# Kernel tuning notes

Measured on AMD Instinct MI355X. Metric: run time of the kernel, lower is better.

## Reference

```python
import jax, jax.numpy as jnp
import numpy as np

B, N, K, C = 4, 8192, 16, 64
HID, OUT = 128, 128


def setup_inputs() -> dict:
    key = jax.random.key(0)
    ks = jax.random.split(key, 8)
    f = jax.random.normal(ks[0], (B, N, C), dtype=jnp.float32)
    knn_idx = jax.random.randint(ks[1], (B, N, K), 0, N, dtype=jnp.int32)
    W1 = jax.random.normal(ks[2], (3 * C, HID), dtype=jnp.float32) * (1.0 / np.sqrt(3 * C))
    b1 = jnp.zeros((HID,), dtype=jnp.float32)
    W2 = jax.random.normal(ks[3], (HID, HID), dtype=jnp.float32) * (1.0 / np.sqrt(HID))
    b2 = jnp.zeros((HID,), dtype=jnp.float32)
    W3 = jax.random.normal(ks[4], (HID, OUT), dtype=jnp.float32) * 0.05  # init.normal_(std=0.05)
    b3 = jnp.zeros((OUT,), dtype=jnp.float32)  # init.zeros_
    return {"f": f, "knn_idx": knn_idx, "W1": W1, "b1": b1, "W2": W2, "b2": b2, "W3": W3, "b3": b3}


def reference(f, knn_idx, W1, b1, W2, b2, W3, b3):
    # knn_group: gather neighbor features -> [B, N, k, C]
    knn_feat = jax.vmap(lambda fb, ib: fb[ib])(f, knn_idx)
    f_tiled = jnp.broadcast_to(f[:, :, None, :], knn_feat.shape)  # [B,N,k,C]
    x = jnp.concatenate([f_tiled, knn_feat, knn_feat - f_tiled], axis=-1)  # [B,N,k,3C]
    x = jax.nn.relu(jnp.einsum('bnkc,ch->bnkh', x, W1) + b1)
    x = jax.nn.relu(jnp.einsum('bnkh,hg->bnkg', x, W2) + b2)
    x = jnp.max(x, axis=2)  # max-pool over k -> [B,N,HID]
    return jnp.einsum('bnh,ho->bno', x, W3) + b3
```

## Files before the change

### kernel.cpp

```cpp
#include <hip/hip_runtime.h>


#define BB 4
#define NN 8192
#define KK 16
#define CC 64
#define HH 128

typedef _Float16 f16;
typedef __fp16 h16x2 __attribute__((ext_vector_type(2)));
typedef _Float16 f16x8 __attribute__((ext_vector_type(8)));
typedef float f32x4 __attribute__((ext_vector_type(4)));

#define MFMA16(a, b, c) __builtin_amdgcn_mfma_f32_16x16x32_f16(a, b, c, 0, 0, 0)

static __device__ __forceinline__ f16x8 cvt8(f32x4 a0, f32x4 a1) {
  h16x2 c0 = __builtin_amdgcn_cvt_pkrtz(a0[0], a0[1]);
  h16x2 c1 = __builtin_amdgcn_cvt_pkrtz(a0[2], a0[3]);
  h16x2 c2 = __builtin_amdgcn_cvt_pkrtz(a1[0], a1[1]);
  h16x2 c3 = __builtin_amdgcn_cvt_pkrtz(a1[2], a1[3]);
  f16x8 v;
  v[0] = (f16)c0[0]; v[1] = (f16)c0[1]; v[2] = (f16)c1[0]; v[3] = (f16)c1[1];
  v[4] = (f16)c2[0]; v[5] = (f16)c2[1]; v[6] = (f16)c3[0]; v[7] = (f16)c3[1];
  return v;
}

static __device__ __forceinline__ void lds_barrier() {
  asm volatile("s_waitcnt lgkmcnt(0)" ::: "memory");
  __builtin_amdgcn_s_barrier();
  __builtin_amdgcn_sched_barrier(0);
}

__global__ void prep_pack(const float* __restrict__ W1, const float* __restrict__ W2,
                          const float* __restrict__ W3, f16* __restrict__ ws) {
  int fid = blockIdx.x * 8 + (threadIdx.x >> 6);
  int l = threadIdx.x & 63;
  int g = l >> 4, r = l & 15;
  f16x8 v;
#pragma unroll
  for (int j = 0; j < 8; ++j) {
    int kl = 16 * (j >> 2) + 4 * g + (j & 3);
    float x;
    if (fid < 16) {
      int ht = fid >> 1, kt = fid & 1, h = ht * 16 + r, k = kt * 32 + kl;
      x = W1[(64 + k) * HH + h] + W1[(128 + k) * HH + h];
    } else if (fid < 48) {
      int t = fid - 16, h2t = t >> 2, kt = t & 3;
      x = W2[(kt * 32 + kl) * HH + h2t * 16 + r];
    } else if (fid < 64) {
      int t = fid - 48, ht = t >> 1, kt = t & 1, h = ht * 16 + r, k = kt * 32 + kl;
      x = W1[k * HH + h] - W1[(128 + k) * HH + h];
    } else {
      int t = fid - 64, ot = t >> 2, kt = t & 3;
      x = W3[(kt * 32 + kl) * HH + ot * 16 + r];
    }
    v[j] = (f16)x;
  }
  *(f16x8*)(ws + (size_t)fid * 512 + l * 8) = v;
}

__global__ void prep_f16(const float* __restrict__ f, f16* __restrict__ fh) {
  int chunk = blockIdx.x * 256 + threadIdx.x;
  int row = chunk >> 3;
  int kt = (chunk >> 2) & 1;
  int g = chunk & 3;
  const float* src = f + (size_t)row * CC + kt * 32;
  f32x4 a0 = *(const f32x4*)(src + 4 * g);
  f32x4 a1 = *(const f32x4*)(src + 16 + 4 * g);
  f16x8 v;
#pragma unroll
  for (int j = 0; j < 4; ++j) { v[j] = (f16)a0[j]; v[4 + j] = (f16)a1[j]; }
  *(f16x8*)(fh + (size_t)row * CC + kt * 32 + g * 8) = v;
}

template <bool F16G>
__global__ __launch_bounds__(512, 4) void knn_main(
    const float* __restrict__ f, const int* __restrict__ knn,
    const float* __restrict__ b1, const float* __restrict__ b2,
    const float* __restrict__ b3, const f16* __restrict__ ws,
    const f16* __restrict__ fh, float* __restrict__ out) {
  extern __shared__ char smem[];
  f16* wbuf = (f16*)smem;
  float* fabuf = (float*)(wbuf + 48 * 512);
  f16* pooled = (f16*)(fabuf + 16 * 132);

  const int tid = threadIdx.x;
  const int wave = tid >> 6, lane = tid & 63;
  const int g = lane >> 4, r = lane & 15;

  const int wg = (blockIdx.x & 7) * 256 + (blockIdx.x >> 3);
  const int b = wg >> 9;
  const int n0 = (wg & 511) * 16;
  const float* fb = f + (size_t)b * NN * CC;
  const f16* fhb = fh + (size_t)b * NN * CC;
  const int p0 = wave * 2;

  int nidx[2];
#pragma unroll
  for (int pp = 0; pp < 2; ++pp)
    nidx[pp] = knn[(size_t)(b * NN + n0 + p0 + pp) * KK + r];

  f16x8 bfa[2];
  f32x4 rawF[2][2];
  if constexpr (F16G) {
    const f16* fo16 = fhb + (size_t)(n0 + r) * CC;
    bfa[0] = *(const f16x8*)(fo16 + g * 8);
    bfa[1] = *(const f16x8*)(fo16 + 32 + g * 8);
  } else {
    const float* fo = fb + (size_t)(n0 + r) * CC;
#pragma unroll
    for (int kt = 0; kt < 2; ++kt) {
      rawF[kt][0] = *(const f32x4*)(fo + kt * 32 + 4 * g);
      rawF[kt][1] = *(const f32x4*)(fo + kt * 32 + 4 * g + 16);
    }
  }
  f16x8 aw[2];
#pragma unroll
  for (int kt = 0; kt < 2; ++kt)
    aw[kt] = *(const f16x8*)(ws + (size_t)(48 + wave * 2 + kt) * 512 + lane * 8);

  f16x8 st[6];
#pragma unroll
  for (int i = 0; i < 6; ++i)
    st[i] = *(const f16x8*)(ws + (size_t)(i * 512 + tid) * 8);
#pragma unroll
  for (int i = 0; i < 6; ++i)
    *(f16x8*)(wbuf + (size_t)(i * 512 + tid) * 8) = st[i];

  f16x8 bf[2][2];
  f32x4 rawN[2][2][2];
  if constexpr (F16G) {
#pragma unroll
    for (int pp = 0; pp < 2; ++pp) {
      const f16* fn16 = fhb + (size_t)nidx[pp] * CC;
#pragma unroll
      for (int kt = 0; kt < 2; ++kt)
        bf[pp][kt] = *(const f16x8*)(fn16 + kt * 32 + g * 8);
    }
  } else {
#pragma unroll
    for (int pp = 0; pp < 2; ++pp) {
      const float* fn = fb + (size_t)nidx[pp] * CC;
#pragma unroll
      for (int kt = 0; kt < 2; ++kt) {
        rawN[pp][kt][0] = *(const f32x4*)(fn + kt * 32 + 4 * g);
        rawN[pp][kt][1] = *(const f32x4*)(fn + kt * 32 + 4 * g + 16);
      }
    }
  }

  {
    f32x4 acc = {0.f, 0.f, 0.f, 0.f};
    if constexpr (F16G) {
      acc = MFMA16(aw[0], bfa[0], acc);
      acc = MFMA16(aw[1], bfa[1], acc);
    } else {
#pragma unroll
      for (int kt = 0; kt < 2; ++kt) {
        f16x8 bfa2 = cvt8(rawF[kt][0], rawF[kt][1]);
        acc = MFMA16(aw[kt], bfa2, acc);
      }
    }
    f32x4 b1v = *(const f32x4*)(b1 + wave * 16 + g * 4);
    f32x4 fa;
#pragma unroll
    for (int i = 0; i < 4; ++i) fa[i] = acc[i] + b1v[i];
    *(f32x4*)(fabuf + r * 132 + wave * 16 + g * 4) = fa;
  }

  lds_barrier();

  if constexpr (!F16G) {
#pragma unroll
    for (int pp = 0; pp < 2; ++pp)
#pragma unroll
      for (int kt = 0; kt < 2; ++kt)
        bf[pp][kt] = cvt8(rawN[pp][kt][0], rawN[pp][kt][1]);
  }

  f16x8 h1f[2][4];
#pragma unroll
  for (int ht = 0; ht < 8; ++ht) {
    f32x4 acc[2] = {{0.f, 0.f, 0.f, 0.f}, {0.f, 0.f, 0.f, 0.f}};
#pragma unroll
    for (int kt = 0; kt < 2; ++kt) {
      f16x8 wfrag = *(const f16x8*)(wbuf + (size_t)(ht * 2 + kt) * 512 + lane * 8);
      acc[0] = MFMA16(wfrag, bf[0][kt], acc[0]);
      acc[1] = MFMA16(wfrag, bf[1][kt], acc[1]);
    }
    f32x4 fa0 = *(const f32x4*)(fabuf + (p0 + 0) * 132 + ht * 16 + g * 4);
    f32x4 fa1 = *(const f32x4*)(fabuf + (p0 + 1) * 132 + ht * 16 + g * 4);
#pragma unroll
    for (int pp = 0; pp < 2; ++pp) {
      const f32x4& fa = pp ? fa1 : fa0;
      float x0 = acc[pp][0] + fa[0]; x0 = x0 > 0.f ? x0 : 0.f;
      float x1 = acc[pp][1] + fa[1]; x1 = x1 > 0.f ? x1 : 0.f;
      float x2 = acc[pp][2] + fa[2]; x2 = x2 > 0.f ? x2 : 0.f;
      float x3 = acc[pp][3] + fa[3]; x3 = x3 > 0.f ? x3 : 0.f;
      h16x2 lo = __builtin_amdgcn_cvt_pkrtz(x0, x1);
      h16x2 hi = __builtin_amdgcn_cvt_pkrtz(x2, x3);
      h1f[pp][ht >> 1][(ht & 1) * 4 + 0] = (f16)lo[0];
      h1f[pp][ht >> 1][(ht & 1) * 4 + 1] = (f16)lo[1];
      h1f[pp][ht >> 1][(ht & 1) * 4 + 2] = (f16)hi[0];
      h1f[pp][ht >> 1][(ht & 1) * 4 + 3] = (f16)hi[1];
    }
  }

#pragma unroll
  for (int h2t = 0; h2t < 8; ++h2t) {
    f32x4 c0 = {0.f, 0.f, 0.f, 0.f}, c1 = {0.f, 0.f, 0.f, 0.f};
#pragma unroll
    for (int kt = 0; kt < 4; ++kt) {
      f16x8 w2f = *(const f16x8*)(wbuf + (size_t)(16 + h2t * 4 + kt) * 512 + lane * 8);
      c0 = MFMA16(h1f[0][kt], w2f, c0);
      c1 = MFMA16(h1f[1][kt], w2f, c1);
    }
    float b2v = b2[h2t * 16 + r];
#pragma unroll
    for (int pp = 0; pp < 2; ++pp) {
      f32x4 cc = pp ? c1 : c0;
      float m = fmaxf(fmaxf(cc[0], cc[1]), fmaxf(cc[2], cc[3]));
      m = fmaxf(m, __shfl_xor(m, 16, 64));
      m = fmaxf(m, __shfl_xor(m, 32, 64));
      float x = m + b2v;
      f16 pv = (f16)(x > 0.f ? x : 0.f);
      if (g == 0) {
        pooled[(h2t >> 1) * 512 + ((r >> 2) * 16 + p0 + pp) * 8 +
               (h2t & 1) * 4 + (r & 3)] = pv;
      }
    }
  }

  f16x8 w3f[4];
#pragma unroll
  for (int kt = 0; kt < 4; ++kt)
    w3f[kt] = *(const f16x8*)(ws + (size_t)(64 + wave * 4 + kt) * 512 + lane * 8);

  lds_barrier();

  {
    f32x4 a3 = {0.f, 0.f, 0.f, 0.f};
#pragma unroll
    for (int kt = 0; kt < 4; ++kt) {
      f16x8 pf = *(const f16x8*)(pooled + kt * 512 + lane * 8);
      a3 = MFMA16(w3f[kt], pf, a3);
    }
    f32x4 b3v = *(const f32x4*)(b3 + wave * 16 + g * 4);
    f32x4 o;
#pragma unroll
    for (int i = 0; i < 4; ++i) o[i] = a3[i] + b3v[i];
    *(f32x4*)(out + ((size_t)b * NN + n0 + r) * HH + wave * 16 + g * 4) = o;
  }
}

extern "C" void kernel_launch(void* const* d_in, const int* in_sizes, int n_in,
                              void* d_out, int out_size, void* d_ws, size_t ws_size,
                              hipStream_t stream) {
  const float* f = (const float*)d_in[0];
  const int* knn = (const int*)d_in[1];
  const float* W1 = (const float*)d_in[2];
  const float* b1 = (const float*)d_in[3];
  const float* W2 = (const float*)d_in[4];
  const float* b2 = (const float*)d_in[5];
  const float* W3 = (const float*)d_in[6];
  const float* b3 = (const float*)d_in[7];
  float* outp = (float*)d_out;
  f16* wsp = (f16*)d_ws;
  f16* fh = wsp + 96 * 512;

  const size_t need = 96 * 1024 + (size_t)BB * NN * CC * 2;

  prep_pack<<<12, 512, 0, stream>>>(W1, W2, W3, wsp);

  if (ws_size >= need) {
    (void)hipFuncSetAttribute((const void*)knn_main<true>,
                              hipFuncAttributeMaxDynamicSharedMemorySize, 61696);
    prep_f16<<<(BB * NN * 8) / 256, 256, 0, stream>>>(f, fh);
    knn_main<true><<<(BB * NN) / 16, 512, 61696, stream>>>(f, knn, b1, b2, b3,
                                                           wsp, fh, outp);
  } else {
    (void)hipFuncSetAttribute((const void*)knn_main<false>,
                              hipFuncAttributeMaxDynamicSharedMemorySize, 61696);
    knn_main<false><<<(BB * NN) / 16, 512, 61696, stream>>>(f, knn, b1, b2, b3,
                                                            wsp, fh, outp);
  }
}
```

Before: 48.99 us.

## Merge prep kernels and make main kernel loop over four tiles with prefetch

Fuses the weight-packing and f16-conversion prep kernels into one launch, cutting one kernel launch. The main kernel now processes four 16-point tiles per workgroup instead of one. It loads weights into LDS once per workgroup and keeps W3 fragments in registers. It also prefetches the next tile's knn indices and gathered features while the current tile's layer-2 and pooling work runs. The trade-off is fewer workgroups (512 instead of 2048) and extra register pressure from the prefetched fragments, which could hurt occupancy or load balance.

```diff
diff --git a/kernel.cpp b/kernel.cpp
--- a/kernel.cpp
+++ b/kernel.cpp
@@ -6,6 +6,7 @@
 #define KK 16
 #define CC 64
 #define HH 128
+#define ITERS 4
 
 typedef _Float16 f16;
 typedef __fp16 h16x2 __attribute__((ext_vector_type(2)));
@@ -31,54 +32,54 @@
   __builtin_amdgcn_sched_barrier(0);
 }
 
-__global__ void prep_pack(const float* __restrict__ W1, const float* __restrict__ W2,
-                          const float* __restrict__ W3, f16* __restrict__ ws) {
-  int fid = blockIdx.x * 8 + (threadIdx.x >> 6);
-  int l = threadIdx.x & 63;
-  int g = l >> 4, r = l & 15;
-  f16x8 v;
-#pragma unroll
-  for (int j = 0; j < 8; ++j) {
-    int kl = 16 * (j >> 2) + 4 * g + (j & 3);
-    float x;
-    if (fid < 16) {
-      int ht = fid >> 1, kt = fid & 1, h = ht * 16 + r, k = kt * 32 + kl;
-      x = W1[(64 + k) * HH + h] + W1[(128 + k) * HH + h];
-    } else if (fid < 48) {
-      int t = fid - 16, h2t = t >> 2, kt = t & 3;
-      x = W2[(kt * 32 + kl) * HH + h2t * 16 + r];
-    } else if (fid < 64) {
-      int t = fid - 48, ht = t >> 1, kt = t & 1, h = ht * 16 + r, k = kt * 32 + kl;
-      x = W1[k * HH + h] - W1[(128 + k) * HH + h];
-    } else {
-      int t = fid - 64, ot = t >> 2, kt = t & 3;
-      x = W3[(kt * 32 + kl) * HH + ot * 16 + r];
-    }
-    v[j] = (f16)x;
-  }
-  *(f16x8*)(ws + (size_t)fid * 512 + l * 8) = v;
-}
-
-__global__ void prep_f16(const float* __restrict__ f, f16* __restrict__ fh) {
-  int chunk = blockIdx.x * 256 + threadIdx.x;
-  int row = chunk >> 3;
-  int kt = (chunk >> 2) & 1;
-  int g = chunk & 3;
-  const float* src = f + (size_t)row * CC + kt * 32;
-  f32x4 a0 = *(const f32x4*)(src + 4 * g);
-  f32x4 a1 = *(const f32x4*)(src + 16 + 4 * g);
-  f16x8 v;
-#pragma unroll
-  for (int j = 0; j < 4; ++j) { v[j] = (f16)a0[j]; v[4 + j] = (f16)a1[j]; }
-  *(f16x8*)(fh + (size_t)row * CC + kt * 32 + g * 8) = v;
-}
-
-template <bool F16G>
-__global__ __launch_bounds__(512, 4) void knn_main(
-    const float* __restrict__ f, const int* __restrict__ knn,
-    const float* __restrict__ b1, const float* __restrict__ b2,
-    const float* __restrict__ b3, const f16* __restrict__ ws,
-    const f16* __restrict__ fh, float* __restrict__ out) {
+__global__ void prep_all(const float* __restrict__ f, const float* __restrict__ W1,
+                         const float* __restrict__ W2, const float* __restrict__ W3,
+                         f16* __restrict__ ws, f16* __restrict__ fh) {
+  if (blockIdx.x < 12) {
+    int fid = blockIdx.x * 8 + (threadIdx.x >> 6);
+    int l = threadIdx.x & 63;
+    int g = l >> 4, r = l & 15;
+    f16x8 v;
+#pragma unroll
+    for (int j = 0; j < 8; ++j) {
+      int kl = 16 * (j >> 2) + 4 * g + (j & 3);
+      float x;
+      if (fid < 16) {
+        int ht = fid >> 1, kt = fid & 1, h = ht * 16 + r, k = kt * 32 + kl;
+        x = W1[(64 + k) * HH + h] + W1[(128 + k) * HH + h];
+      } else if (fid < 48) {
+        int t = fid - 16, h2t = t >> 2, kt = t & 3;
+        x = W2[(kt * 32 + kl) * HH + h2t * 16 + r];
+      } else if (fid < 64) {
+        int t = fid - 48, ht = t >> 1, kt = t & 1, h = ht * 16 + r, k = kt * 32 + kl;
+        x = W1[k * HH + h] - W1[(128 + k) * HH + h];
+      } else {
+        int t = fid - 64, ot = t >> 2, kt = t & 3;
+        x = W3[(kt * 32 + kl) * HH + ot * 16 + r];
+      }
+      v[j] = (f16)x;
+    }
+    *(f16x8*)(ws + (size_t)fid * 512 + l * 8) = v;
+  } else {
+    int chunk = (blockIdx.x - 12) * 512 + threadIdx.x;
+    int row = chunk >> 3;
+    int kt = (chunk >> 2) & 1;
+    int g = chunk & 3;
+    const float* src = f + (size_t)row * CC + kt * 32;
+    f32x4 a0 = *(const f32x4*)(src + 4 * g);
+    f32x4 a1 = *(const f32x4*)(src + 16 + 4 * g);
+    f16x8 v;
+#pragma unroll
+    for (int j = 0; j < 4; ++j) { v[j] = (f16)a0[j]; v[4 + j] = (f16)a1[j]; }
+    *(f16x8*)(fh + (size_t)row * CC + kt * 32 + g * 8) = v;
+  }
+}
+
+__global__ __launch_bounds__(512, 4) void knn_pers(
+    const int* __restrict__ knn, const float* __restrict__ b1,
+    const float* __restrict__ b2, const float* __restrict__ b3,
+    const f16* __restrict__ ws, const f16* __restrict__ fh,
+    float* __restrict__ out) {
   extern __shared__ char smem[];
   f16* wbuf = (f16*)smem;
   float* fabuf = (float*)(wbuf + 48 * 512);
@@ -88,11 +89,179 @@
   const int wave = tid >> 6, lane = tid & 63;
   const int g = lane >> 4, r = lane & 15;
 
+  const int wg = (blockIdx.x & 7) * 64 + (blockIdx.x >> 3);
+  const int b = wg >> 7;
+  const int nbase = (wg & 127) * 64;
+  const f16* fhb = fh + (size_t)b * NN * CC;
+  const int p0 = wave * 2;
+
+  f16x8 st[6];
+#pragma unroll
+  for (int i = 0; i < 6; ++i)
+    st[i] = *(const f16x8*)(ws + (size_t)(i * 512 + tid) * 8);
+#pragma unroll
+  for (int i = 0; i < 6; ++i)
+    *(f16x8*)(wbuf + (size_t)(i * 512 + tid) * 8) = st[i];
+
+  f16x8 aw[2], w3f[4];
+#pragma unroll
+  for (int kt = 0; kt < 2; ++kt)
+    aw[kt] = *(const f16x8*)(ws + (size_t)(48 + wave * 2 + kt) * 512 + lane * 8);
+#pragma unroll
+  for (int kt = 0; kt < 4; ++kt)
+    w3f[kt] = *(const f16x8*)(ws + (size_t)(64 + wave * 4 + kt) * 512 + lane * 8);
+
+  int nidx[2];
+#pragma unroll
+  for (int pp = 0; pp < 2; ++pp)
+    nidx[pp] = knn[(size_t)(b * NN + nbase + p0 + pp) * KK + r];
+  f16x8 bfa[2];
+  {
+    const f16* fo16 = fhb + (size_t)(nbase + r) * CC;
+    bfa[0] = *(const f16x8*)(fo16 + g * 8);
+    bfa[1] = *(const f16x8*)(fo16 + 32 + g * 8);
+  }
+  f16x8 bf[2][2];
+#pragma unroll
+  for (int pp = 0; pp < 2; ++pp) {
+    const f16* fn16 = fhb + (size_t)nidx[pp] * CC;
+#pragma unroll
+    for (int kt = 0; kt < 2; ++kt)
+      bf[pp][kt] = *(const f16x8*)(fn16 + kt * 32 + g * 8);
+  }
+
+  for (int it = 0; it < ITERS; ++it) {
+    const int n0 = nbase + it * 16;
+    const int itn = (it < ITERS - 1) ? it + 1 : it;
+
+    int nidxN[2];
+#pragma unroll
+    for (int pp = 0; pp < 2; ++pp)
+      nidxN[pp] = knn[(size_t)(b * NN + nbase + itn * 16 + p0 + pp) * KK + r];
+
+    {
+      f32x4 acc = {0.f, 0.f, 0.f, 0.f};
+      acc = MFMA16(aw[0], bfa[0], acc);
+      acc = MFMA16(aw[1], bfa[1], acc);
+      f32x4 b1v = *(const f32x4*)(b1 + wave * 16 + g * 4);
+      f32x4 fa;
+#pragma unroll
+      for (int i = 0; i < 4; ++i) fa[i] = acc[i] + b1v[i];
+      *(f32x4*)(fabuf + r * 132 + wave * 16 + g * 4) = fa;
+    }
+
+    lds_barrier();
+
+    f16x8 h1f[2][4];
+#pragma unroll
+    for (int ht = 0; ht < 8; ++ht) {
+      f32x4 acc[2] = {{0.f, 0.f, 0.f, 0.f}, {0.f, 0.f, 0.f, 0.f}};
+#pragma unroll
+      for (int kt = 0; kt < 2; ++kt) {
+        f16x8 wfrag = *(const f16x8*)(wbuf + (size_t)(ht * 2 + kt) * 512 + lane * 8);
+        acc[0] = MFMA16(wfrag, bf[0][kt], acc[0]);
+        acc[1] = MFMA16(wfrag, bf[1][kt], acc[1]);
+      }
+      f32x4 fa0 = *(const f32x4*)(fabuf + (p0 + 0) * 132 + ht * 16 + g * 4);
+      f32x4 fa1 = *(const f32x4*)(fabuf + (p0 + 1) * 132 + ht * 16 + g * 4);
+#pragma unroll
+      for (int pp = 0; pp < 2; ++pp) {
+        const f32x4& fa = pp ? fa1 : fa0;
+        float x0 = acc[pp][0] + fa[0]; x0 = x0 > 0.f ? x0 : 0.f;
+        float x1 = acc[pp][1] + fa[1]; x1 = x1 > 0.f ? x1 : 0.f;
+        float x2 = acc[pp][2] + fa[2]; x2 = x2 > 0.f ? x2 : 0.f;
+        float x3 = acc[pp][3] + fa[3]; x3 = x3 > 0.f ? x3 : 0.f;
+        h16x2 lo = __builtin_amdgcn_cvt_pkrtz(x0, x1);
+        h16x2 hi = __builtin_amdgcn_cvt_pkrtz(x2, x3);
+        h1f[pp][ht >> 1][(ht & 1) * 4 + 0] = (f16)lo[0];
+        h1f[pp][ht >> 1][(ht & 1) * 4 + 1] = (f16)lo[1];
+        h1f[pp][ht >> 1][(ht & 1) * 4 + 2] = (f16)hi[0];
+        h1f[pp][ht >> 1][(ht & 1) * 4 + 3] = (f16)hi[1];
+      }
+    }
+
+#pragma unroll
+    for (int h2t = 0; h2t < 8; ++h2t) {
+      f32x4 c0 = {0.f, 0.f, 0.f, 0.f}, c1 = {0.f, 0.f, 0.f, 0.f};
+#pragma unroll
+      for (int kt = 0; kt < 4; ++kt) {
+        f16x8 w2f = *(const f16x8*)(wbuf + (size_t)(16 + h2t * 4 + kt) * 512 + lane * 8);
+        c0 = MFMA16(h1f[0][kt], w2f, c0);
+        c1 = MFMA16(h1f[1][kt], w2f, c1);
+      }
+      float b2v = b2[h2t * 16 + r];
+#pragma unroll
+      for (int pp = 0; pp < 2; ++pp) {
+        f32x4 cc = pp ? c1 : c0;
+        float m = fmaxf(fmaxf(cc[0], cc[1]), fmaxf(cc[2], cc[3]));
+        m = fmaxf(m, __shfl_xor(m, 16, 64));
+        m = fmaxf(m, __shfl_xor(m, 32, 64));
+        float x = m + b2v;
+        f16 pv = (f16)(x > 0.f ? x : 0.f);
+        if (g == 0) {
+          pooled[(h2t >> 1) * 512 + ((r >> 2) * 16 + p0 + pp) * 8 +
+                 (h2t & 1) * 4 + (r & 3)] = pv;
+        }
+      }
+    }
+
+    f16x8 bfaN[2], bfN[2][2];
+    {
+      const f16* fo16 = fhb + (size_t)(nbase + itn * 16 + r) * CC;
+      bfaN[0] = *(const f16x8*)(fo16 + g * 8);
+      bfaN[1] = *(const f16x8*)(fo16 + 32 + g * 8);
+    }
+#pragma unroll
+    for (int pp = 0; pp < 2; ++pp) {
+      const f16* fn16 = fhb + (size_t)nidxN[pp] * CC;
+#pragma unroll
+      for (int kt = 0; kt < 2; ++kt)
+        bfN[pp][kt] = *(const f16x8*)(fn16 + kt * 32 + g * 8);
+    }
+
+    lds_barrier();
+
+    {
+      f32x4 a3 = {0.f, 0.f, 0.f, 0.f};
+#pragma unroll
+      for (int kt = 0; kt < 4; ++kt) {
+        f16x8 pf = *(const f16x8*)(pooled + kt * 512 + lane * 8);
+        a3 = MFMA16(w3f[kt], pf, a3);
+      }
+      f32x4 b3v = *(const f32x4*)(b3 + wave * 16 + g * 4);
+      f32x4 o;
+#pragma unroll
+      for (int i = 0; i < 4; ++i) o[i] = a3[i] + b3v[i];
+      *(f32x4*)(out + ((size_t)b * NN + n0 + r) * HH + wave * 16 + g * 4) = o;
+    }
+
+    bfa[0] = bfaN[0]; bfa[1] = bfaN[1];
+#pragma unroll
+    for (int pp = 0; pp < 2; ++pp)
+#pragma unroll
+      for (int kt = 0; kt < 2; ++kt)
+        bf[pp][kt] = bfN[pp][kt];
+    nidx[0] = nidxN[0]; nidx[1] = nidxN[1];
+  }
+}
+
+__global__ __launch_bounds__(512, 4) void knn_fb(
+    const float* __restrict__ f, const int* __restrict__ knn,
+    const float* __restrict__ b1, const float* __restrict__ b2,
+    const float* __restrict__ b3, const f16* __restrict__ ws,
+    float* __restrict__ out) {
+  extern __shared__ char smem[];
+  f16* wbuf = (f16*)smem;
+  float* fabuf = (float*)(wbuf + 48 * 512);
+  f16* pooled = (f16*)(fabuf + 16 * 132);
+
+  const int tid = threadIdx.x;
+  const int wave = tid >> 6, lane = tid & 63;
+  const int g = lane >> 4, r = lane & 15;
   const int wg = (blockIdx.x & 7) * 256 + (blockIdx.x >> 3);
   const int b = wg >> 9;
   const int n0 = (wg & 511) * 16;
   const float* fb = f + (size_t)b * NN * CC;
-  const f16* fhb = fh + (size_t)b * NN * CC;
   const int p0 = wave * 2;
 
   int nidx[2];
@@ -100,19 +269,12 @@
   for (int pp = 0; pp < 2; ++pp)
     nidx[pp] = knn[(size_t)(b * NN + n0 + p0 + pp) * KK + r];
 
-  f16x8 bfa[2];
+  const float* fo = fb + (size_t)(n0 + r) * CC;
   f32x4 rawF[2][2];
-  if constexpr (F16G) {
-    const f16* fo16 = fhb + (size_t)(n0 + r) * CC;
-    bfa[0] = *(const f16x8*)(fo16 + g * 8);
-    bfa[1] = *(const f16x8*)(fo16 + 32 + g * 8);
-  } else {
-    const float* fo = fb + (size_t)(n0 + r) * CC;
-#pragma unroll
-    for (int kt = 0; kt < 2; ++kt) {
-      rawF[kt][0] = *(const f32x4*)(fo + kt * 32 + 4 * g);
-      rawF[kt][1] = *(const f32x4*)(fo + kt * 32 + 4 * g + 16);
-    }
+#pragma unroll
+  for (int kt = 0; kt < 2; ++kt) {
+    rawF[kt][0] = *(const f32x4*)(fo + kt * 32 + 4 * g);
+    rawF[kt][1] = *(const f32x4*)(fo + kt * 32 + 4 * g + 16);
   }
   f16x8 aw[2];
 #pragma unroll
@@ -127,39 +289,23 @@
   for (int i = 0; i < 6; ++i)
     *(f16x8*)(wbuf + (size_t)(i * 512 + tid) * 8) = st[i];
 
-  f16x8 bf[2][2];
   f32x4 rawN[2][2][2];
-  if constexpr (F16G) {
-#pragma unroll
-    for (int pp = 0; pp < 2; ++pp) {
-      const f16* fn16 = fhb + (size_t)nidx[pp] * CC;
-#pragma unroll
-      for (int kt = 0; kt < 2; ++kt)
-        bf[pp][kt] = *(const f16x8*)(fn16 + kt * 32 + g * 8);
-    }
-  } else {
-#pragma unroll
-    for (int pp = 0; pp < 2; ++pp) {
-      const float* fn = fb + (size_t)nidx[pp] * CC;
-#pragma unroll
-      for (int kt = 0; kt < 2; ++kt) {
-        rawN[pp][kt][0] = *(const f32x4*)(fn + kt * 32 + 4 * g);
-        rawN[pp][kt][1] = *(const f32x4*)(fn + kt * 32 + 4 * g + 16);
-      }
+#pragma unroll
+  for (int pp = 0; pp < 2; ++pp) {
+    const float* fn = fb + (size_t)nidx[pp] * CC;
+#pragma unroll
+    for (int kt = 0; kt < 2; ++kt) {
+      rawN[pp][kt][0] = *(const f32x4*)(fn + kt * 32 + 4 * g);
+      rawN[pp][kt][1] = *(const f32x4*)(fn + kt * 32 + 4 * g + 16);
     }
   }
 
   {
     f32x4 acc = {0.f, 0.f, 0.f, 0.f};
-    if constexpr (F16G) {
-      acc = MFMA16(aw[0], bfa[0], acc);
-      acc = MFMA16(aw[1], bfa[1], acc);
-    } else {
-#pragma unroll
-      for (int kt = 0; kt < 2; ++kt) {
-        f16x8 bfa2 = cvt8(rawF[kt][0], rawF[kt][1]);
-        acc = MFMA16(aw[kt], bfa2, acc);
-      }
+#pragma unroll
+    for (int kt = 0; kt < 2; ++kt) {
+      f16x8 bfa2 = cvt8(rawF[kt][0], rawF[kt][1]);
+      acc = MFMA16(aw[kt], bfa2, acc);
     }
     f32x4 b1v = *(const f32x4*)(b1 + wave * 16 + g * 4);
     f32x4 fa;
@@ -170,13 +316,12 @@
 
   lds_barrier();
 
-  if constexpr (!F16G) {
-#pragma unroll
-    for (int pp = 0; pp < 2; ++pp)
-#pragma unroll
-      for (int kt = 0; kt < 2; ++kt)
-        bf[pp][kt] = cvt8(rawN[pp][kt][0], rawN[pp][kt][1]);
-  }
+  f16x8 bf[2][2];
+#pragma unroll
+  for (int pp = 0; pp < 2; ++pp)
+#pragma unroll
+    for (int kt = 0; kt < 2; ++kt)
+      bf[pp][kt] = cvt8(rawN[pp][kt][0], rawN[pp][kt][1]);
 
   f16x8 h1f[2][4];
 #pragma unroll
@@ -270,18 +415,15 @@
 
   const size_t need = 96 * 1024 + (size_t)BB * NN * CC * 2;
 
-  prep_pack<<<12, 512, 0, stream>>>(W1, W2, W3, wsp);
-
   if (ws_size >= need) {
-    (void)hipFuncSetAttribute((const void*)knn_main<true>,
+    (void)hipFuncSetAttribute((const void*)knn_pers,
                               hipFuncAttributeMaxDynamicSharedMemorySize, 61696);
-    prep_f16<<<(BB * NN * 8) / 256, 256, 0, stream>>>(f, fh);
-    knn_main<true><<<(BB * NN) / 16, 512, 61696, stream>>>(f, knn, b1, b2, b3,
-                                                           wsp, fh, outp);
+    prep_all<<<12 + (BB * NN * 8) / 512, 512, 0, stream>>>(f, W1, W2, W3, wsp, fh);
+    knn_pers<<<(BB * NN) / 64, 512, 61696, stream>>>(knn, b1, b2, b3, wsp, fh, outp);
   } else {
-    (void)hipFuncSetAttribute((const void*)knn_main<false>,
+    (void)hipFuncSetAttribute((const void*)knn_fb,
                               hipFuncAttributeMaxDynamicSharedMemorySize, 61696);
-    knn_main<false><<<(BB * NN) / 16, 512, 61696, stream>>>(f, knn, b1, b2, b3,
-                                                            wsp, fh, outp);
-  }
-}
+    prep_all<<<12, 512, 0, stream>>>(f, W1, W2, W3, wsp, fh);
+    knn_fb<<<(BB * NN) / 16, 512, 61696, stream>>>(f, knn, b1, b2, b3, wsp, outp);
+  }
+}
```

Result: faster. 44.71 us (-8.7%).
